# Kernel tuning notes

Hardware: AMD Instinct MI355X
Metric: run time of the kernel (lower is better)

Reference implementation:

```python
import jax, jax.numpy as jnp
import numpy as np

B, S, L = 8, 2048, 8
H, NH = 768, 12
DH = H // NH
NUM_REL = 100
LN_EPS = 1e-5


def setup_inputs() -> dict:
    key = jax.random.key(0)
    ks = jax.random.split(key, 16)
    inp = {
        'text_embeddings': jax.random.normal(ks[0], (B, S, H), dtype=jnp.float32),
        # values in [-1, 64); -1 marks 'no leaf' and is masked out
        'graph_structure': jax.random.randint(ks[1], (B, S, L), -1, 64, dtype=jnp.int64),
        'relation_ids': jax.random.randint(ks[2], (B, S, L), 0, NUM_REL, dtype=jnp.int64),
        'rel_table': jax.random.normal(ks[3], (NUM_REL, H), dtype=jnp.float32),
        'Wq': jax.random.normal(ks[4], (H, H), dtype=jnp.float32) / np.sqrt(H),
        'bq': jnp.zeros((H,), dtype=jnp.float32),
        'Wk': jax.random.normal(ks[5], (H, H), dtype=jnp.float32) / np.sqrt(H),
        'bk': jnp.zeros((H,), dtype=jnp.float32),
        'Wv': jax.random.normal(ks[6], (H, H), dtype=jnp.float32) / np.sqrt(H),
        'bv': jnp.zeros((H,), dtype=jnp.float32),
        'Wo': jax.random.normal(ks[7], (H, H), dtype=jnp.float32) / np.sqrt(H),
        'bo': jnp.zeros((H,), dtype=jnp.float32),
        'gamma': jnp.ones((H,), dtype=jnp.float32),
        'beta': jnp.zeros((H,), dtype=jnp.float32),
    }
    return inp


def reference(text_embeddings, graph_structure, relation_ids, rel_table,
              Wq, bq, Wk, bk, Wv, bv, Wo, bo, gamma, beta):
    b, s, h = text_embeddings.shape
    l = relation_ids.shape[2]
    # embedding gather (clamp -1 -> 0, masked later)
    rel_emb = rel_table[jnp.clip(relation_ids, 0, None)]  # [B,S,L,H]
    # projections; query has length-1 per root token
    q = (text_embeddings @ Wq + bq).reshape(b, s, NH, DH)          # [B,S,N,D]
    k = (rel_emb @ Wk + bk).reshape(b, s, l, NH, DH)               # [B,S,L,N,D]
    v = (rel_emb @ Wv + bv).reshape(b, s, l, NH, DH)
    scores = jnp.einsum('bsnd,bslnd->bsnl', q, k) / np.sqrt(DH)    # [B,S,N,L]
    mask = (graph_structure != -1)[:, :, None, :]                  # [B,S,1,L]
    scores = jnp.where(mask, scores, jnp.float32(-10000.0))
    probs = jax.nn.softmax(scores, axis=-1)                        # [B,S,N,L]
    ctx = jnp.einsum('bsnl,bslnd->bsnd', probs, v).reshape(b, s, h)
    out = ctx @ Wo + bo
    x = text_embeddings + out
    mu = jnp.mean(x, axis=-1, keepdims=True)
    var = jnp.mean(jnp.square(x - mu), axis=-1, keepdims=True)
    return (x - mu) * jax.lax.rsqrt(var + LN_EPS) * gamma + beta
```

## Files before the change

### kernel.cpp

```cpp
#include <hip/hip_runtime.h>
#include <hip/hip_bf16.h>

#define H 768
#define NH 12
#define DH 64
#define LL 8
#define NTOK 16384
#define NREL 100
#define NRELP 128
#define PADW 72

typedef __attribute__((ext_vector_type(8))) short short8;
typedef __attribute__((ext_vector_type(4))) float f32x4;

__device__ __forceinline__ float bf2f(ushort u) {
  union { unsigned int i; float f; } v; v.i = ((unsigned int)u) << 16; return v.f;
}
__device__ __forceinline__ float bflo(unsigned int u) {
  union { unsigned int i; float f; } v; v.i = u << 16; return v.f;
}
__device__ __forceinline__ float bfhi(unsigned int u) {
  union { unsigned int i; float f; } v; v.i = u & 0xffff0000u; return v.f;
}
__device__ __forceinline__ ushort f2bf(float f) {
  union { float f; unsigned int i; } v; v.f = f;
  unsigned int x = v.i;
  return (ushort)((x + 0x7fffu + ((x >> 16) & 1u)) >> 16);
}
__device__ __forceinline__ unsigned int cvt_pk_bf16(float lo, float hi) {
  unsigned int r;
  asm("v_cvt_pk_bf16_f32 %0, %1, %2" : "=v"(r) : "v"(lo), "v"(hi));
  return r;
}

__global__ __launch_bounds__(256) void prep_kernel(
    const float* __restrict__ s0, ushort* __restrict__ d0,
    const float* __restrict__ s1, ushort* __restrict__ d1,
    const float* __restrict__ s2, ushort* __restrict__ d2,
    const float* __restrict__ s3, ushort* __restrict__ d3,
    const float* __restrict__ rel, ushort* __restrict__ RelB) {
  if (blockIdx.z == 4) {
    int b = blockIdx.y * 24 + blockIdx.x;
    if (b < 96) {
      int i = (b * 256 + threadIdx.x) * 4;
      int row = i / H;
      ushort4 o = {0, 0, 0, 0};
      if (row < NREL) {
        float4 v = *(const float4*)(rel + i);
        o.x = f2bf(v.x); o.y = f2bf(v.y); o.z = f2bf(v.z); o.w = f2bf(v.w);
      }
      *(ushort4*)(RelB + i) = o;
    }
    return;
  }
  const float* src; ushort* dst;
  switch (blockIdx.z) {
    case 0:  src = s0; dst = d0; break;
    case 1:  src = s1; dst = d1; break;
    case 2:  src = s2; dst = d2; break;
    default: src = s3; dst = d3; break;
  }
  __shared__ float tile[32][33];
  int bx = blockIdx.x * 32, by = blockIdx.y * 32;
  int tx = threadIdx.x & 31, ty = threadIdx.x >> 5;
  #pragma unroll
  for (int i = 0; i < 32; i += 8)
    tile[ty + i][tx] = src[(size_t)(by + ty + i) * H + bx + tx];
  __syncthreads();
  #pragma unroll
  for (int i = 0; i < 32; i += 8)
    dst[(size_t)(bx + ty + i) * H + by + tx] = f2bf(tile[tx][ty + i]);
}

__device__ __forceinline__ void gload_lds16(const void* g, void* l) {
  __builtin_amdgcn_global_load_lds(
      (const __attribute__((address_space(1))) unsigned int*)g,
      (__attribute__((address_space(3))) unsigned int*)l, 16, 0, 0);
}

#define BM 64
#define BN 128
#define BK 64

#define GEMM_COMPUTE()                                                         \
  _Pragma("unroll")                                                            \
  for (int kk = 0; kk < 2; ++kk) {                                             \
    const int sw = (((kk << 2) | lk) ^ (lr & 7)) * 8;                          \
    short8 af[2], bfr[4];                                                      \
    _Pragma("unroll")                                                          \
    for (int m = 0; m < 2; ++m)                                                \
      af[m] = *(const short8*)(As + (wr * 32 + m * 16 + lr) * BK + sw);        \
    _Pragma("unroll")                                                          \
    for (int n = 0; n < 4; ++n)                                                \
      bfr[n] = *(const short8*)(Bs + (wc * 64 + n * 16 + lr) * BK + sw);       \
    _Pragma("unroll")                                                          \
    for (int m = 0; m < 2; ++m)                                                \
      _Pragma("unroll")                                                        \
      for (int n = 0; n < 4; ++n)                                              \
        acc[m][n] = __builtin_amdgcn_mfma_f32_16x16x32_bf16(af[m], bfr[n],     \
                                                            acc[m][n], 0, 0, 0);\
  }

#define GEMM_EPILOGUE()                                                        \
  _Pragma("unroll")                                                            \
  for (int m = 0; m < 2; ++m) {                                                \
    _Pragma("unroll")                                                          \
    for (int n = 0; n < 4; ++n) {                                              \
      int col = col0 + wc * 64 + n * 16 + lr;                                  \
      float b = bias[col];                                                     \
      _Pragma("unroll")                                                        \
      for (int j = 0; j < 4; ++j) {                                            \
        int row = row0 + wr * 32 + m * 16 + lk * 4 + j;                        \
        C[(size_t)row * N + col] = f2bf(acc[m][n][j] + b);                     \
      }                                                                        \
    }                                                                          \
  }

__device__ __forceinline__ void gemm_body(
    ushort* As, ushort* Bs,
    const ushort* __restrict__ A,
    const ushort* __restrict__ Bt,
    const float* __restrict__ bias,
    ushort* __restrict__ C,
    int M, int N, int K, int bx, int by) {
  const int tid = threadIdx.x;
  const int row0 = by * BM;
  const int col0 = bx * BN;
  const int wave = tid >> 6;
  const int lane = tid & 63;
  const int wr = wave >> 1, wc = wave & 1;
  const int lr = lane & 15, lk = lane >> 4;
  f32x4 acc[2][4];
  #pragma unroll
  for (int m = 0; m < 2; ++m)
    #pragma unroll
    for (int n = 0; n < 4; ++n) acc[m][n] = (f32x4)(0.f);

  for (int k0 = 0; k0 < K; k0 += BK) {
    #pragma unroll
    for (int i = 0; i < 2; ++i) {
      int c = tid + i * 256;
      int r = c >> 3, s = c & 7;
      int gs = s ^ (r & 7);
      gload_lds16(A + (size_t)(row0 + r) * K + k0 + gs * 8, (char*)As + c * 16);
    }
    #pragma unroll
    for (int i = 0; i < 4; ++i) {
      int c = tid + i * 256;
      int r = c >> 3, s = c & 7;
      int gs = s ^ (r & 7);
      gload_lds16(Bt + (size_t)(col0 + r) * K + k0 + gs * 8, (char*)Bs + c * 16);
    }
    __syncthreads();
    GEMM_COMPUTE()
    __syncthreads();
  }
  GEMM_EPILOGUE()
}

__device__ __forceinline__ void gemm_body_a32(
    ushort* As, ushort* Bs,
    const float* __restrict__ A32,
    const ushort* __restrict__ Bt,
    const float* __restrict__ bias,
    ushort* __restrict__ C,
    int M, int N, int K, int bx, int by) {
  const int tid = threadIdx.x;
  const int row0 = by * BM;
  const int col0 = bx * BN;
  const int wave = tid >> 6;
  const int lane = tid & 63;
  const int wr = wave >> 1, wc = wave & 1;
  const int lr = lane & 15, lk = lane >> 4;
  f32x4 acc[2][4];
  #pragma unroll
  for (int m = 0; m < 2; ++m)
    #pragma unroll
    for (int n = 0; n < 4; ++n) acc[m][n] = (f32x4)(0.f);

  for (int k0 = 0; k0 < K; k0 += BK) {
    #pragma unroll
    for (int i = 0; i < 4; ++i) {
      int c = tid + i * 256;
      int r = c >> 3, s = c & 7;
      int gs = s ^ (r & 7);
      gload_lds16(Bt + (size_t)(col0 + r) * K + k0 + gs * 8, (char*)Bs + c * 16);
    }
    #pragma unroll
    for (int i = 0; i < 2; ++i) {
      int c = tid + i * 256;
      int r = c >> 3, s = c & 7;
      int gs = s ^ (r & 7);
      const float* src = A32 + (size_t)(row0 + r) * K + k0 + gs * 8;
      float4 f0 = *(const float4*)(src);
      float4 f1 = *(const float4*)(src + 4);
      uint4 w;
      w.x = cvt_pk_bf16(f0.x, f0.y);
      w.y = cvt_pk_bf16(f0.z, f0.w);
      w.z = cvt_pk_bf16(f1.x, f1.y);
      w.w = cvt_pk_bf16(f1.z, f1.w);
      *(uint4*)((char*)As + c * 16) = w;
    }
    __syncthreads();
    GEMM_COMPUTE()
    __syncthreads();
  }
  GEMM_EPILOGUE()
}

__global__ __launch_bounds__(256, 4) void gemm_q_kv_kernel(
    const float* __restrict__ X, const ushort* __restrict__ WqT,
    const float* __restrict__ bq, ushort* __restrict__ Qbf,
    const ushort* __restrict__ RelB,
    const ushort* __restrict__ WkT, const float* __restrict__ bk, ushort* __restrict__ Ktab,
    const ushort* __restrict__ WvT, const float* __restrict__ bv, ushort* __restrict__ Vtab) {
  __shared__ ushort As[BM * BK];
  __shared__ ushort Bs[BN * BK];
  int lin = blockIdx.x;
  if (lin < 24) {
    if (lin < 12)
      gemm_body(As, Bs, RelB, WkT, bk, Ktab, NRELP, H, H, lin % 6, lin / 6);
    else {
      int l = lin - 12;
      gemm_body(As, Bs, RelB, WvT, bv, Vtab, NRELP, H, H, l % 6, l / 6);
    }
    return;
  }
  int l2 = lin - 24;
  int wg = (l2 & 7) * 192 + (l2 >> 3);
  gemm_body_a32(As, Bs, X, WqT, bq, Qbf, NTOK, H, H, wg % 6, wg / 6);
}

__global__ __launch_bounds__(256, 4) void gemm_bt_kernel(
    const ushort* __restrict__ A, const ushort* __restrict__ Bt,
    const float* __restrict__ bias, ushort* __restrict__ C,
    int M, int N, int K) {
  __shared__ ushort As[BM * BK];
  __shared__ ushort Bs[BN * BK];
  int lin = blockIdx.y * gridDim.x + blockIdx.x;
  int q = (gridDim.x * gridDim.y) >> 3;
  int wg = (lin & 7) * q + (lin >> 3);
  gemm_body(As, Bs, A, Bt, bias, C, M, N, K, wg % gridDim.x, wg / gridDim.x);
}

__global__ __launch_bounds__(256) void attn3_kernel(
    const ushort* __restrict__ Q,
    const ushort* __restrict__ Ktab,
    const ushort* __restrict__ Vtab,
    const int* __restrict__ graph,
    const int* __restrict__ relid,
    ushort* __restrict__ Ctx) {
  __shared__ __align__(16) ushort Ks[NREL * PADW];
  __shared__ __align__(16) ushort Vs[NREL * PADW];
  const int tid = threadIdx.x;
  const int head = blockIdx.y;
  const int t = blockIdx.x * 256 + tid;

  #pragma unroll
  for (int i = 0; i < 4; ++i) {
    int c = tid + i * 256;
    if (c < NREL * 9) {
      int row = c / 9, slot = c - row * 9;
      int gs = (slot < 8) ? slot * 8 : 0;
      const size_t src = (size_t)row * H + head * DH + gs;
      gload_lds16(Ktab + src, (char*)Ks + (size_t)c * 16);
      gload_lds16(Vtab + src, (char*)Vs + (size_t)c * 16);
    }
  }

  const uint4* qp = (const uint4*)(Q + (size_t)t * H + head * DH);
  uint4 qw[8];
  #pragma unroll
  for (int j = 0; j < 8; ++j) qw[j] = qp[j];
  const int4* gp = (const int4*)(graph + (size_t)t * LL);
  const int4* rp = (const int4*)(relid + (size_t)t * LL);
  int4 ga = gp[0], gb = gp[1];
  int4 ra = rp[0], rb = rp[1];
  int gs[8] = {ga.x, ga.y, ga.z, ga.w, gb.x, gb.y, gb.z, gb.w};
  int rid[8] = {ra.x, ra.y, ra.z, ra.w, rb.x, rb.y, rb.z, rb.w};
  int koff[8];
  #pragma unroll
  for (int l = 0; l < 8; ++l) {
    int r = rid[l] < 0 ? 0 : rid[l];
    koff[l] = r * (PADW * 2);
  }

  __syncthreads();

  float s[8];
  #pragma unroll
  for (int l = 0; l < 8; ++l) s[l] = 0.f;
  #pragma unroll
  for (int j = 0; j < 8; ++j) {
    float qf[8];
    qf[0] = bflo(qw[j].x); qf[1] = bfhi(qw[j].x);
    qf[2] = bflo(qw[j].y); qf[3] = bfhi(qw[j].y);
    qf[4] = bflo(qw[j].z); qf[5] = bfhi(qw[j].z);
    qf[6] = bflo(qw[j].w); qf[7] = bfhi(qw[j].w);
    #pragma unroll
    for (int l = 0; l < 8; ++l) {
      uint4 kw = *(const uint4*)((const char*)Ks + koff[l] + j * 16);
      s[l] += qf[0] * bflo(kw.x) + qf[1] * bfhi(kw.x)
            + qf[2] * bflo(kw.y) + qf[3] * bfhi(kw.y)
            + qf[4] * bflo(kw.z) + qf[5] * bfhi(kw.z)
            + qf[6] * bflo(kw.w) + qf[7] * bfhi(kw.w);
    }
  }

  #pragma unroll
  for (int l = 0; l < 8; ++l)
    s[l] = (gs[l] != -1) ? s[l] * 0.125f : -10000.0f;
  float mx = s[0];
  #pragma unroll
  for (int l = 1; l < 8; ++l) mx = fmaxf(mx, s[l]);
  float p[8], den = 0.f;
  #pragma unroll
  for (int l = 0; l < 8; ++l) { p[l] = __expf(s[l] - mx); den += p[l]; }
  float inv = 1.f / den;
  #pragma unroll
  for (int l = 0; l < 8; ++l) p[l] *= inv;

  ushort* cp = Ctx + (size_t)t * H + head * DH;
  #pragma unroll
  for (int j = 0; j < 8; ++j) {
    float a[8];
    #pragma unroll
    for (int d = 0; d < 8; ++d) a[d] = 0.f;
    #pragma unroll
    for (int l = 0; l < 8; ++l) {
      uint4 vw = *(const uint4*)((const char*)Vs + koff[l] + j * 16);
      a[0] += p[l] * bflo(vw.x); a[1] += p[l] * bfhi(vw.x);
      a[2] += p[l] * bflo(vw.y); a[3] += p[l] * bfhi(vw.y);
      a[4] += p[l] * bflo(vw.z); a[5] += p[l] * bfhi(vw.z);
      a[6] += p[l] * bflo(vw.w); a[7] += p[l] * bfhi(vw.w);
    }
    short8 o;
    #pragma unroll
    for (int d = 0; d < 8; ++d) o[d] = (short)f2bf(a[d]);
    *(short8*)(cp + j * 8) = o;
  }
}

__global__ __launch_bounds__(192) void ln_kernel(
    const float* __restrict__ text, const ushort* __restrict__ op,
    const float* __restrict__ gamma, const float* __restrict__ beta,
    float* __restrict__ out) {
  int t = blockIdx.x;
  int c0 = threadIdx.x * 4;
  float4 tv = *(const float4*)(text + (size_t)t * H + c0);
  ushort4 ov = *(const ushort4*)(op + (size_t)t * H + c0);
  float x0 = tv.x + bf2f(ov.x), x1 = tv.y + bf2f(ov.y);
  float x2 = tv.z + bf2f(ov.z), x3 = tv.w + bf2f(ov.w);
  float s = x0 + x1 + x2 + x3;
  float s2 = x0 * x0 + x1 * x1 + x2 * x2 + x3 * x3;
  #pragma unroll
  for (int off = 32; off > 0; off >>= 1) {
    s  += __shfl_xor(s, off, 64);
    s2 += __shfl_xor(s2, off, 64);
  }
  __shared__ float red[2][3];
  int wave = threadIdx.x >> 6, lane = threadIdx.x & 63;
  if (lane == 0) { red[0][wave] = s; red[1][wave] = s2; }
  __syncthreads();
  s  = red[0][0] + red[0][1] + red[0][2];
  s2 = red[1][0] + red[1][1] + red[1][2];
  float mu = s * (1.f / H);
  float var = s2 * (1.f / H) - mu * mu;
  float rs = rsqrtf(var + 1e-5f);
  float4 g4 = *(const float4*)(gamma + c0);
  float4 b4 = *(const float4*)(beta + c0);
  float4 o4;
  o4.x = (x0 - mu) * rs * g4.x + b4.x;
  o4.y = (x1 - mu) * rs * g4.y + b4.y;
  o4.z = (x2 - mu) * rs * g4.z + b4.z;
  o4.w = (x3 - mu) * rs * g4.w + b4.w;
  *(float4*)(out + (size_t)t * H + c0) = o4;
}

extern "C" void kernel_launch(void* const* d_in, const int* in_sizes, int n_in,
                              void* d_out, int out_size, void* d_ws, size_t ws_size,
                              hipStream_t stream) {
  const float* text      = (const float*)d_in[0];
  const int*   graph     = (const int*)d_in[1];
  const int*   relid     = (const int*)d_in[2];
  const float* rel_table = (const float*)d_in[3];
  const float* Wq = (const float*)d_in[4];  const float* bq = (const float*)d_in[5];
  const float* Wk = (const float*)d_in[6];  const float* bk = (const float*)d_in[7];
  const float* Wv = (const float*)d_in[8];  const float* bv = (const float*)d_in[9];
  const float* Wo = (const float*)d_in[10]; const float* bo = (const float*)d_in[11];
  const float* gamma = (const float*)d_in[12];
  const float* beta  = (const float*)d_in[13];
  float* out = (float*)d_out;
  char* ws = (char*)d_ws;

  const size_t TOKH = (size_t)NTOK * H;
  size_t off = 0;
  ushort* Ctx  = (ushort*)(ws + off); off += TOKH * 2;
  ushort* Qbf  = (ushort*)(ws + off); off += TOKH * 2;
  ushort* WqT  = (ushort*)(ws + off); off += (size_t)H * H * 2;
  ushort* WoT  = (ushort*)(ws + off); off += (size_t)H * H * 2;
  ushort* WkT  = (ushort*)(ws + off); off += (size_t)H * H * 2;
  ushort* WvT  = (ushort*)(ws + off); off += (size_t)H * H * 2;
  ushort* RelB = (ushort*)(ws + off); off += (size_t)NRELP * H * 2;
  ushort* Ktab = (ushort*)(ws + off); off += (size_t)NRELP * H * 2;
  ushort* Vtab = (ushort*)(ws + off); off += (size_t)NRELP * H * 2;

  prep_kernel<<<dim3(24, 24, 5), 256, 0, stream>>>(
      Wq, WqT, Wo, WoT, Wk, WkT, Wv, WvT, rel_table, RelB);
  gemm_q_kv_kernel<<<24 + 1536, 256, 0, stream>>>(
      text, WqT, bq, Qbf, RelB, WkT, bk, Ktab, WvT, bv, Vtab);
  dim3 ga(NTOK / 256, NH);
  attn3_kernel<<<ga, 256, 0, stream>>>(Qbf, Ktab, Vtab, graph, relid, Ctx);
  dim3 g1(H / BN, NTOK / BM);
  gemm_bt_kernel<<<g1, 256, 0, stream>>>(Ctx, WoT, bo, Qbf, NTOK, H, H);
  ln_kernel<<<NTOK, 192, 0, stream>>>(text, Qbf, gamma, beta, out);
}
```

Before: 113.6 us.

## Double-buffer LDS tiles in GEMM bodies to overlap loads with MFMA

Converts both GEMM bodies to a double-buffered LDS pipeline: the next K tile is prefetched (via global_load_lds for bf16, register loads plus deferred conversion for fp32 A) while MFMAs run on the current buffer. This leaves one barrier per K step instead of two. In exchange, LDS use doubles and the launch-bounds occupancy hint drops from 4 to 3 blocks per CU.

New measurement: 121.8 us. 7.2% more time.

```diff
diff --git a/kernel.cpp b/kernel.cpp
--- a/kernel.cpp
+++ b/kernel.cpp
@@ -81,18 +81,20 @@
 #define BM 64
 #define BN 128
 #define BK 64
-
-#define GEMM_COMPUTE()                                                         \
+#define ATILE (BM * BK)
+#define BTILE (BN * BK)
+
+#define GEMM_COMPUTE(cb)                                                       \
   _Pragma("unroll")                                                            \
   for (int kk = 0; kk < 2; ++kk) {                                             \
     const int sw = (((kk << 2) | lk) ^ (lr & 7)) * 8;                          \
     short8 af[2], bfr[4];                                                      \
     _Pragma("unroll")                                                          \
     for (int m = 0; m < 2; ++m)                                                \
-      af[m] = *(const short8*)(As + (wr * 32 + m * 16 + lr) * BK + sw);        \
+      af[m] = *(const short8*)(As + (cb) * ATILE + (wr * 32 + m * 16 + lr) * BK + sw); \
     _Pragma("unroll")                                                          \
     for (int n = 0; n < 4; ++n)                                                \
-      bfr[n] = *(const short8*)(Bs + (wc * 64 + n * 16 + lr) * BK + sw);       \
+      bfr[n] = *(const short8*)(Bs + (cb) * BTILE + (wc * 64 + n * 16 + lr) * BK + sw); \
     _Pragma("unroll")                                                          \
     for (int m = 0; m < 2; ++m)                                                \
       _Pragma("unroll")                                                        \
@@ -136,24 +138,38 @@
     #pragma unroll
     for (int n = 0; n < 4; ++n) acc[m][n] = (f32x4)(0.f);
 
-  for (int k0 = 0; k0 < K; k0 += BK) {
-    #pragma unroll
-    for (int i = 0; i < 2; ++i) {
-      int c = tid + i * 256;
-      int r = c >> 3, s = c & 7;
-      int gs = s ^ (r & 7);
-      gload_lds16(A + (size_t)(row0 + r) * K + k0 + gs * 8, (char*)As + c * 16);
-    }
-    #pragma unroll
-    for (int i = 0; i < 4; ++i) {
-      int c = tid + i * 256;
-      int r = c >> 3, s = c & 7;
-      int gs = s ^ (r & 7);
-      gload_lds16(Bt + (size_t)(col0 + r) * K + k0 + gs * 8, (char*)Bs + c * 16);
-    }
+  const int nt = K / BK;
+  #pragma unroll
+  for (int i = 0; i < 2; ++i) {
+    int c = tid + i * 256; int r = c >> 3, s = c & 7; int gsx = s ^ (r & 7);
+    gload_lds16(A + (size_t)(row0 + r) * K + gsx * 8, (char*)As + c * 16);
+  }
+  #pragma unroll
+  for (int i = 0; i < 4; ++i) {
+    int c = tid + i * 256; int r = c >> 3, s = c & 7; int gsx = s ^ (r & 7);
+    gload_lds16(Bt + (size_t)(col0 + r) * K + gsx * 8, (char*)Bs + c * 16);
+  }
+  __syncthreads();
+  int cb = 0;
+  for (int t = 0; t < nt; ++t) {
+    if (t + 1 < nt) {
+      int k1 = (t + 1) * BK;
+      #pragma unroll
+      for (int i = 0; i < 2; ++i) {
+        int c = tid + i * 256; int r = c >> 3, s = c & 7; int gsx = s ^ (r & 7);
+        gload_lds16(A + (size_t)(row0 + r) * K + k1 + gsx * 8,
+                    (char*)As + (cb ^ 1) * (ATILE * 2) + c * 16);
+      }
+      #pragma unroll
+      for (int i = 0; i < 4; ++i) {
+        int c = tid + i * 256; int r = c >> 3, s = c & 7; int gsx = s ^ (r & 7);
+        gload_lds16(Bt + (size_t)(col0 + r) * K + k1 + gsx * 8,
+                    (char*)Bs + (cb ^ 1) * (BTILE * 2) + c * 16);
+      }
+    }
+    GEMM_COMPUTE(cb)
     __syncthreads();
-    GEMM_COMPUTE()
-    __syncthreads();
+    cb ^= 1;
   }
   GEMM_EPILOGUE()
 }
@@ -178,44 +194,72 @@
     #pragma unroll
     for (int n = 0; n < 4; ++n) acc[m][n] = (f32x4)(0.f);
 
-  for (int k0 = 0; k0 < K; k0 += BK) {
-    #pragma unroll
-    for (int i = 0; i < 4; ++i) {
-      int c = tid + i * 256;
-      int r = c >> 3, s = c & 7;
-      int gs = s ^ (r & 7);
-      gload_lds16(Bt + (size_t)(col0 + r) * K + k0 + gs * 8, (char*)Bs + c * 16);
-    }
-    #pragma unroll
-    for (int i = 0; i < 2; ++i) {
-      int c = tid + i * 256;
-      int r = c >> 3, s = c & 7;
-      int gs = s ^ (r & 7);
-      const float* src = A32 + (size_t)(row0 + r) * K + k0 + gs * 8;
-      float4 f0 = *(const float4*)(src);
-      float4 f1 = *(const float4*)(src + 4);
+  const int nt = K / BK;
+  #pragma unroll
+  for (int i = 0; i < 4; ++i) {
+    int c = tid + i * 256; int r = c >> 3, s = c & 7; int gsx = s ^ (r & 7);
+    gload_lds16(Bt + (size_t)(col0 + r) * K + gsx * 8, (char*)Bs + c * 16);
+  }
+  #pragma unroll
+  for (int i = 0; i < 2; ++i) {
+    int c = tid + i * 256; int r = c >> 3, s = c & 7; int gsx = s ^ (r & 7);
+    const float* src = A32 + (size_t)(row0 + r) * K + gsx * 8;
+    float4 f0 = *(const float4*)(src);
+    float4 f1 = *(const float4*)(src + 4);
+    uint4 w;
+    w.x = cvt_pk_bf16(f0.x, f0.y);
+    w.y = cvt_pk_bf16(f0.z, f0.w);
+    w.z = cvt_pk_bf16(f1.x, f1.y);
+    w.w = cvt_pk_bf16(f1.z, f1.w);
+    *(uint4*)((char*)As + c * 16) = w;
+  }
+  __syncthreads();
+  int cb = 0;
+  for (int t = 0; t < nt; ++t) {
+    float4 fa0, fa1, fb0, fb1;
+    if (t + 1 < nt) {
+      int k1 = (t + 1) * BK;
+      #pragma unroll
+      for (int i = 0; i < 4; ++i) {
+        int c = tid + i * 256; int r = c >> 3, s = c & 7; int gsx = s ^ (r & 7);
+        gload_lds16(Bt + (size_t)(col0 + r) * K + k1 + gsx * 8,
+                    (char*)Bs + (cb ^ 1) * (BTILE * 2) + c * 16);
+      }
+      {
+        int c = tid;            int r = c >> 3, s = c & 7; int gsx = s ^ (r & 7);
+        const float* src = A32 + (size_t)(row0 + r) * K + k1 + gsx * 8;
+        fa0 = *(const float4*)(src); fa1 = *(const float4*)(src + 4);
+      }
+      {
+        int c = tid + 256;      int r = c >> 3, s = c & 7; int gsx = s ^ (r & 7);
+        const float* src = A32 + (size_t)(row0 + r) * K + k1 + gsx * 8;
+        fb0 = *(const float4*)(src); fb1 = *(const float4*)(src + 4);
+      }
+    }
+    GEMM_COMPUTE(cb)
+    if (t + 1 < nt) {
       uint4 w;
-      w.x = cvt_pk_bf16(f0.x, f0.y);
-      w.y = cvt_pk_bf16(f0.z, f0.w);
-      w.z = cvt_pk_bf16(f1.x, f1.y);
-      w.w = cvt_pk_bf16(f1.z, f1.w);
-      *(uint4*)((char*)As + c * 16) = w;
+      w.x = cvt_pk_bf16(fa0.x, fa0.y); w.y = cvt_pk_bf16(fa0.z, fa0.w);
+      w.z = cvt_pk_bf16(fa1.x, fa1.y); w.w = cvt_pk_bf16(fa1.z, fa1.w);
+      *(uint4*)((char*)As + (cb ^ 1) * (ATILE * 2) + tid * 16) = w;
+      w.x = cvt_pk_bf16(fb0.x, fb0.y); w.y = cvt_pk_bf16(fb0.z, fb0.w);
+      w.z = cvt_pk_bf16(fb1.x, fb1.y); w.w = cvt_pk_bf16(fb1.z, fb1.w);
+      *(uint4*)((char*)As + (cb ^ 1) * (ATILE * 2) + (tid + 256) * 16) = w;
     }
     __syncthreads();
-    GEMM_COMPUTE()
-    __syncthreads();
+    cb ^= 1;
   }
   GEMM_EPILOGUE()
 }
 
-__global__ __launch_bounds__(256, 4) void gemm_q_kv_kernel(
+__global__ __launch_bounds__(256, 3) void gemm_q_kv_kernel(
     const float* __restrict__ X, const ushort* __restrict__ WqT,
     const float* __restrict__ bq, ushort* __restrict__ Qbf,
     const ushort* __restrict__ RelB,
     const ushort* __restrict__ WkT, const float* __restrict__ bk, ushort* __restrict__ Ktab,
     const ushort* __restrict__ WvT, const float* __restrict__ bv, ushort* __restrict__ Vtab) {
-  __shared__ ushort As[BM * BK];
-  __shared__ ushort Bs[BN * BK];
+  __shared__ ushort As[2 * ATILE];
+  __shared__ ushort Bs[2 * BTILE];
   int lin = blockIdx.x;
   if (lin < 24) {
     if (lin < 12)
@@ -231,12 +275,12 @@
   gemm_body_a32(As, Bs, X, WqT, bq, Qbf, NTOK, H, H, wg % 6, wg / 6);
 }
 
-__global__ __launch_bounds__(256, 4) void gemm_bt_kernel(
+__global__ __launch_bounds__(256, 3) void gemm_bt_kernel(
     const ushort* __restrict__ A, const ushort* __restrict__ Bt,
     const float* __restrict__ bias, ushort* __restrict__ C,
     int M, int N, int K) {
-  __shared__ ushort As[BM * BK];
-  __shared__ ushort Bs[BN * BK];
+  __shared__ ushort As[2 * ATILE];
+  __shared__ ushort Bs[2 * BTILE];
   int lin = blockIdx.y * gridDim.x + blockIdx.x;
   int q = (gridDim.x * gridDim.y) >> 3;
   int wg = (lin & 7) * q + (lin >> 3);
@@ -261,8 +305,8 @@
     int c = tid + i * 256;
     if (c < NREL * 9) {
       int row = c / 9, slot = c - row * 9;
-      int gs = (slot < 8) ? slot * 8 : 0;
-      const size_t src = (size_t)row * H + head * DH + gs;
+      int gsx = (slot < 8) ? slot * 8 : 0;
+      const size_t src = (size_t)row * H + head * DH + gsx;
       gload_lds16(Ktab + src, (char*)Ks + (size_t)c * 16);
       gload_lds16(Vtab + src, (char*)Vs + (size_t)c * 16);
     }
```
